# Kernel tuning notes

Hardware: AMD Instinct MI355X
Metric: run time of the kernel (lower is better)

The kernel has to match this reference:

```python
import jax, jax.numpy as jnp
import numpy as np

ROUTING_ITERS = 3
EPS = 1e-8

def _squash_elem(s):
    # Faithful to torch squash with dim=-1 over a trailing size-1 axis: elementwise.
    sq = s * s
    return (sq / (1.0 + sq)) * s / jnp.sqrt(sq + EPS)

def setup_inputs() -> dict:
    key = jax.random.key(0)
    k1, k2 = jax.random.split(key)
    x = jax.random.normal(k1, (64, 1152, 64), dtype=jnp.float32)            # [B, N_routes, in_ch]
    route_weights = jax.random.normal(k2, (32, 1152, 64, 64), dtype=jnp.float32)  # [C, N, out, in]
    return {"x": x, "route_weights": route_weights}

def reference(x, route_weights):
    B = x.shape[0]
    C, N, O, _ = route_weights.shape
    # u_hat: [B, C, N, O]  (torch trailing size-1 dim dropped; squash/sums over it are elementwise)
    u_hat = jnp.einsum('cnoi,bni->bcno', route_weights, x)
    b_ij = jnp.zeros((B, C, N, 1), dtype=x.dtype)
    v_j = None
    for i in range(ROUTING_ITERS):
        c_ij = jax.nn.softmax(b_ij, axis=1)                  # over capsules
        s_j = jnp.sum(c_ij * u_hat, axis=2, keepdims=True)   # [B, C, 1, O]
        v_j = _squash_elem(s_j)
        if i < ROUTING_ITERS - 1:
            # torch: b_ij + (u_hat * v_j).sum(-1, keepdim) over size-1 dim -> broadcasts to [B,C,N,O]
            b_ij = b_ij + u_hat * v_j
    return v_j[:, :, 0, :]  # [B, C, O]
```

## Files before the change

### kernel.cpp

```cpp
#include <hip/hip_runtime.h>
#include <hip/hip_bf16.h>

typedef short short8v __attribute__((ext_vector_type(8)));
typedef float float4v __attribute__((ext_vector_type(4)));

constexpr int Bb = 64;
constexpr int Cc = 32;
constexpr int Nn = 1152;
constexpr int Oo = 64;
constexpr int Ii = 64;
constexpr int NCH = 32;
constexpr int CHN = 36;
constexpr int OT  = 16;

__device__ __forceinline__ unsigned short bf16_rne(float f) {
    unsigned u = __float_as_uint(f);
    u += 0x7FFFu + ((u >> 16) & 1u);
    return (unsigned short)(u >> 16);
}
__device__ __forceinline__ float bf16_f(unsigned short h) {
    return __uint_as_float(((unsigned)h) << 16);
}
__device__ __forceinline__ float squash_elem(float s) {
    float sq = s * s;
    return (sq / (1.f + sq)) * s / sqrtf(sq + 1e-8f);
}

__global__ __launch_bounds__(256) void prep_x(const float* __restrict__ x,
                                              unsigned short* __restrict__ xh,
                                              unsigned short* __restrict__ xl) {
    size_t g = (size_t)blockIdx.x * 256 + threadIdx.x;
    float4 v = ((const float4*)x)[g];
    float a[4] = {v.x, v.y, v.z, v.w};
    ushort4 H, L;
    unsigned short* hp = (unsigned short*)&H;
    unsigned short* lp = (unsigned short*)&L;
#pragma unroll
    for (int e = 0; e < 4; ++e) {
        unsigned short hb = bf16_rne(a[e]);
        hp[e] = hb;
        lp[e] = bf16_rne(a[e] - bf16_f(hb));
    }
    ((ushort4*)xh)[g] = H;
    ((ushort4*)xl)[g] = L;
}

template <int MODE>
__global__ __launch_bounds__(256, 2) void caps_pass(
    const float* __restrict__ w, const unsigned short* __restrict__ xh,
    const unsigned short* __restrict__ xl, const float* __restrict__ V,
    float* __restrict__ part) {
    __shared__ unsigned short sh[2][128 * 64];
    __shared__ unsigned short sl[2][128 * 64];

    const int t = threadIdx.x;
    const int l = t & 63, wv = t >> 6;
    const int ch = blockIdx.x, ot = blockIdx.y;
    const int obase = ot * 4;
    const int kg = l >> 4;
    const int lm = l & 15;
    const int n0 = ch * CHN;

    float Vreg[8][4];
    if constexpr (MODE == 1) {
#pragma unroll
        for (int t8 = 0; t8 < 8; ++t8)
#pragma unroll
            for (int r = 0; r < 4; ++r) {
                int b = 16 * wv + 4 * kg + r;
                int c = 4 * t8 + ((l >> 2) & 3);
                int o = obase + (l & 3);
                Vreg[t8][r] = V[((size_t)b * Cc + c) * Oo + o];
            }
    }
    float accs[8][4];
#pragma unroll
    for (int t8 = 0; t8 < 8; ++t8)
#pragma unroll
        for (int r = 0; r < 4; ++r) accs[t8][r] = 0.f;

    const int i0 = (t & 15) * 4;
    const int colb = t >> 4;
    float4 ld[8];

    auto issue = [&](int n) {
#pragma unroll
        for (int k = 0; k < 8; ++k) {
            int col = colb + 16 * k;
            int c = col >> 2, ol = col & 3;
            const float* g =
                w + (((size_t)c * Nn + n) * Oo + obase + ol) * Ii + i0;
            ld[k] = *(const float4*)g;
        }
    };
    auto writebuf = [&](int buf) {
#pragma unroll
        for (int k = 0; k < 8; ++k) {
            int col = colb + 16 * k;
            int off = col * 64 + i0;
            float a[4] = {ld[k].x, ld[k].y, ld[k].z, ld[k].w};
            ushort4 H, L;
            unsigned short* hp = (unsigned short*)&H;
            unsigned short* lp = (unsigned short*)&L;
#pragma unroll
            for (int e = 0; e < 4; ++e) {
                unsigned short hb = bf16_rne(a[e]);
                hp[e] = hb;
                lp[e] = bf16_rne(a[e] - bf16_f(hb));
            }
            *(ushort4*)(&sh[buf][off]) = H;
            *(ushort4*)(&sl[buf][off]) = L;
        }
    };

    issue(n0);
    writebuf(0);
    __syncthreads();

    for (int j = 0; j < CHN; ++j) {
        const int n = n0 + j, cur = j & 1;
        if (j + 1 < CHN) issue(n0 + j + 1);

        const size_t xoff = ((size_t)(16 * wv + lm) * Nn + n) * Ii + kg * 8;
        short8v ah0 = *(const short8v*)(xh + xoff);
        short8v al0 = *(const short8v*)(xl + xoff);
        short8v ah1 = *(const short8v*)(xh + xoff + 32);
        short8v al1 = *(const short8v*)(xl + xoff + 32);

        float u[8][4];
#pragma unroll
        for (int t8 = 0; t8 < 8; ++t8) {
            int coff = (16 * t8 + lm) * 64 + kg * 8;
            short8v bh0 = *(const short8v*)(&sh[cur][coff]);
            short8v bl0 = *(const short8v*)(&sl[cur][coff]);
            short8v bh1 = *(const short8v*)(&sh[cur][coff + 32]);
            short8v bl1 = *(const short8v*)(&sl[cur][coff + 32]);
            float4v a = {0.f, 0.f, 0.f, 0.f};
            a = __builtin_amdgcn_mfma_f32_16x16x32_bf16(ah0, bh0, a, 0, 0, 0);
            a = __builtin_amdgcn_mfma_f32_16x16x32_bf16(al0, bh0, a, 0, 0, 0);
            a = __builtin_amdgcn_mfma_f32_16x16x32_bf16(ah0, bl0, a, 0, 0, 0);
            a = __builtin_amdgcn_mfma_f32_16x16x32_bf16(ah1, bh1, a, 0, 0, 0);
            a = __builtin_amdgcn_mfma_f32_16x16x32_bf16(al1, bh1, a, 0, 0, 0);
            a = __builtin_amdgcn_mfma_f32_16x16x32_bf16(ah1, bl1, a, 0, 0, 0);
            u[t8][0] = a[0]; u[t8][1] = a[1]; u[t8][2] = a[2]; u[t8][3] = a[3];
        }

        if constexpr (MODE == 0) {
#pragma unroll
            for (int t8 = 0; t8 < 8; ++t8)
#pragma unroll
                for (int r = 0; r < 4; ++r) accs[t8][r] += u[t8][r];
        } else {
#pragma unroll
            for (int r = 0; r < 4; ++r) {
                float m = -1e30f;
#pragma unroll
                for (int t8 = 0; t8 < 8; ++t8)
                    m = fmaxf(m, u[t8][r] * Vreg[t8][r]);
                m = fmaxf(m, __shfl_xor(m, 4));
                m = fmaxf(m, __shfl_xor(m, 8));
                float Z = 0.f;
#pragma unroll
                for (int t8 = 0; t8 < 8; ++t8) {
                    float e = __expf(u[t8][r] * Vreg[t8][r] - m);
                    Z += e;
                    u[t8][r] *= e;
                }
                Z += __shfl_xor(Z, 4);
                Z += __shfl_xor(Z, 8);
                float rz = 1.f / Z;
#pragma unroll
                for (int t8 = 0; t8 < 8; ++t8) accs[t8][r] += u[t8][r] * rz;
            }
        }

        if (j + 1 < CHN) {
            writebuf(cur ^ 1);
            __syncthreads();
        }
    }

#pragma unroll
    for (int t8 = 0; t8 < 8; ++t8)
#pragma unroll
        for (int r = 0; r < 4; ++r) {
            int b = 16 * wv + 4 * kg + r;
            int c = 4 * t8 + ((l >> 2) & 3);
            int o = obase + (l & 3);
            part[(((size_t)ch * Bb + b) * Cc + c) * Oo + o] = accs[t8][r];
        }
}

__global__ void reduce_caps(const float* __restrict__ part,
                            float* __restrict__ V, float* __restrict__ out,
                            int mode) {
    int bc = blockIdx.x;
    int o = threadIdx.x;
    size_t base = (size_t)bc * 64 + o;
    float s = 0.f;
    for (int c = 0; c < NCH; ++c) s += part[(size_t)c * (Bb * Cc * Oo) + base];
    if (mode == 0)      V[base] = squash_elem(s * (1.f / 32.f));
    else if (mode == 1) V[base] += squash_elem(s);
    else                out[base] = squash_elem(s);
}

extern "C" void kernel_launch(void* const* d_in, const int* in_sizes, int n_in,
                              void* d_out, int out_size, void* d_ws, size_t ws_size,
                              hipStream_t stream) {
    const float* x = (const float*)d_in[0];
    const float* w = (const float*)d_in[1];
    float* out = (float*)d_out;

    const size_t XE = (size_t)Bb * Nn * Ii;
    unsigned short* xh = (unsigned short*)d_ws;
    unsigned short* xl = xh + XE;
    float* part = (float*)(xl + XE);
    float* V = part + (size_t)NCH * Bb * Cc * Oo;

    prep_x<<<(int)(XE / 4 / 256), 256, 0, stream>>>(x, xh, xl);

    caps_pass<0><<<dim3(NCH, OT), 256, 0, stream>>>(w, xh, xl, nullptr, part);
    reduce_caps<<<Bb * Cc, 64, 0, stream>>>(part, V, out, 0);
    caps_pass<1><<<dim3(NCH, OT), 256, 0, stream>>>(w, xh, xl, V, part);
    reduce_caps<<<Bb * Cc, 64, 0, stream>>>(part, V, out, 1);
    caps_pass<1><<<dim3(NCH, OT), 256, 0, stream>>>(w, xh, xl, V, part);
    reduce_caps<<<Bb * Cc, 64, 0, stream>>>(part, V, out, 2);
}
```

Measured before the change: 509.0 us.

## Swizzle LDS weight tiles, deepen register prefetch, accumulate directly in MFMA

After: 495.3 us. 2.7% less time.

```diff
diff --git a/kernel.cpp b/kernel.cpp
--- a/kernel.cpp
+++ b/kernel.cpp
@@ -12,6 +12,7 @@
 constexpr int NCH = 32;
 constexpr int CHN = 36;
 constexpr int OT  = 16;
+constexpr int COLS = 128;
 
 __device__ __forceinline__ unsigned short bf16_rne(float f) {
     unsigned u = __float_as_uint(f);
@@ -50,8 +51,8 @@
     const float* __restrict__ w, const unsigned short* __restrict__ xh,
     const unsigned short* __restrict__ xl, const float* __restrict__ V,
     float* __restrict__ part) {
-    __shared__ unsigned short sh[2][128 * 64];
-    __shared__ unsigned short sl[2][128 * 64];
+    __shared__ unsigned short sh[2][COLS * 64];
+    __shared__ unsigned short sl[2][COLS * 64];
 
     const int t = threadIdx.x;
     const int l = t & 63, wv = t >> 6;
@@ -60,6 +61,7 @@
     const int kg = l >> 4;
     const int lm = l & 15;
     const int n0 = ch * CHN;
+    const int sw = (lm & 7) << 3;
 
     float Vreg[8][4];
     if constexpr (MODE == 1) {
@@ -73,31 +75,34 @@
                 Vreg[t8][r] = V[((size_t)b * Cc + c) * Oo + o];
             }
     }
+    float4v acc4[8];
     float accs[8][4];
 #pragma unroll
-    for (int t8 = 0; t8 < 8; ++t8)
+    for (int t8 = 0; t8 < 8; ++t8) {
+        acc4[t8] = (float4v){0.f, 0.f, 0.f, 0.f};
 #pragma unroll
         for (int r = 0; r < 4; ++r) accs[t8][r] = 0.f;
+    }
 
     const int i0 = (t & 15) * 4;
     const int colb = t >> 4;
-    float4 ld[8];
-
-    auto issue = [&](int n) {
+    float4 L0[8], L1[8];
+
+    auto issue = [&](int n, float4(&ld)[8]) {
 #pragma unroll
         for (int k = 0; k < 8; ++k) {
             int col = colb + 16 * k;
-            int c = col >> 2, ol = col & 3;
-            const float* g =
-                w + (((size_t)c * Nn + n) * Oo + obase + ol) * Ii + i0;
-            ld[k] = *(const float4*)g;
+            int c = col >> 2, olc = col & 3;
+            ld[k] = *(const float4*)(
+                w + (((size_t)c * Nn + n) * Oo + obase + olc) * Ii + i0);
         }
     };
-    auto writebuf = [&](int buf) {
+    auto writebuf = [&](unsigned short* dh, unsigned short* dl,
+                        const float4(&ld)[8]) {
 #pragma unroll
         for (int k = 0; k < 8; ++k) {
             int col = colb + 16 * k;
-            int off = col * 64 + i0;
+            int off = col * 64 + (i0 ^ ((col & 7) << 3));
             float a[4] = {ld[k].x, ld[k].y, ld[k].z, ld[k].w};
             ushort4 H, L;
             unsigned short* hp = (unsigned short*)&H;
@@ -108,19 +113,12 @@
                 hp[e] = hb;
                 lp[e] = bf16_rne(a[e] - bf16_f(hb));
             }
-            *(ushort4*)(&sh[buf][off]) = H;
-            *(ushort4*)(&sl[buf][off]) = L;
+            *(ushort4*)(dh + off) = H;
+            *(ushort4*)(dl + off) = L;
         }
     };
-
-    issue(n0);
-    writebuf(0);
-    __syncthreads();
-
-    for (int j = 0; j < CHN; ++j) {
-        const int n = n0 + j, cur = j & 1;
-        if (j + 1 < CHN) issue(n0 + j + 1);
-
+    auto compute = [&](const unsigned short* bh_, const unsigned short* bl_,
+                       int n) {
         const size_t xoff = ((size_t)(16 * wv + lm) * Nn + n) * Ii + kg * 8;
         short8v ah0 = *(const short8v*)(xh + xoff);
         short8v al0 = *(const short8v*)(xl + xoff);
@@ -130,27 +128,30 @@
         float u[8][4];
 #pragma unroll
         for (int t8 = 0; t8 < 8; ++t8) {
-            int coff = (16 * t8 + lm) * 64 + kg * 8;
-            short8v bh0 = *(const short8v*)(&sh[cur][coff]);
-            short8v bl0 = *(const short8v*)(&sl[cur][coff]);
-            short8v bh1 = *(const short8v*)(&sh[cur][coff + 32]);
-            short8v bl1 = *(const short8v*)(&sl[cur][coff + 32]);
-            float4v a = {0.f, 0.f, 0.f, 0.f};
+            int row = 16 * t8 + lm;
+            int c0 = row * 64 + ((kg * 8) ^ sw);
+            int c1 = row * 64 + (((kg * 8) + 32) ^ sw);
+            short8v bh0 = *(const short8v*)(bh_ + c0);
+            short8v bl0 = *(const short8v*)(bl_ + c0);
+            short8v bh1 = *(const short8v*)(bh_ + c1);
+            short8v bl1 = *(const short8v*)(bl_ + c1);
+            float4v a;
+            if constexpr (MODE == 0) a = acc4[t8];
+            else a = (float4v){0.f, 0.f, 0.f, 0.f};
             a = __builtin_amdgcn_mfma_f32_16x16x32_bf16(ah0, bh0, a, 0, 0, 0);
             a = __builtin_amdgcn_mfma_f32_16x16x32_bf16(al0, bh0, a, 0, 0, 0);
             a = __builtin_amdgcn_mfma_f32_16x16x32_bf16(ah0, bl0, a, 0, 0, 0);
             a = __builtin_amdgcn_mfma_f32_16x16x32_bf16(ah1, bh1, a, 0, 0, 0);
             a = __builtin_amdgcn_mfma_f32_16x16x32_bf16(al1, bh1, a, 0, 0, 0);
             a = __builtin_amdgcn_mfma_f32_16x16x32_bf16(ah1, bl1, a, 0, 0, 0);
-            u[t8][0] = a[0]; u[t8][1] = a[1]; u[t8][2] = a[2]; u[t8][3] = a[3];
-        }
-
-        if constexpr (MODE == 0) {
-#pragma unroll
-            for (int t8 = 0; t8 < 8; ++t8)
-#pragma unroll
-                for (int r = 0; r < 4; ++r) accs[t8][r] += u[t8][r];
-        } else {
+            if constexpr (MODE == 0) {
+                acc4[t8] = a;
+            } else {
+                u[t8][0] = a[0]; u[t8][1] = a[1];
+                u[t8][2] = a[2]; u[t8][3] = a[3];
+            }
+        }
+        if constexpr (MODE == 1) {
 #pragma unroll
             for (int r = 0; r < 4; ++r) {
                 float m = -1e30f;
@@ -173,11 +174,22 @@
                 for (int t8 = 0; t8 < 8; ++t8) accs[t8][r] += u[t8][r] * rz;
             }
         }
-
-        if (j + 1 < CHN) {
-            writebuf(cur ^ 1);
-            __syncthreads();
-        }
+    };
+
+    issue(n0, L0);
+    writebuf(sh[0], sl[0], L0);
+    issue(n0 + 1, L1);
+    __syncthreads();
+
+    for (int j = 0; j < CHN; j += 2) {
+        writebuf(sh[1], sl[1], L1);
+        if (j + 2 < CHN) issue(n0 + j + 2, L0);
+        compute(sh[0], sl[0], n0 + j);
+        __syncthreads();
+        if (j + 2 < CHN) writebuf(sh[0], sl[0], L0);
+        if (j + 3 < CHN) issue(n0 + j + 3, L1);
+        compute(sh[1], sl[1], n0 + j + 1);
+        __syncthreads();
     }
 
 #pragma unroll
@@ -187,7 +199,8 @@
             int b = 16 * wv + 4 * kg + r;
             int c = 4 * t8 + ((l >> 2) & 3);
             int o = obase + (l & 3);
-            part[(((size_t)ch * Bb + b) * Cc + c) * Oo + o] = accs[t8][r];
+            float val = (MODE == 0) ? acc4[t8][r] : accs[t8][r];
+            part[(((size_t)ch * Bb + b) * Cc + c) * Oo + o] = val;
         }
 }
 
```
